# Kernel tuning notes

Hardware: AMD Instinct MI355X
Metric: run time of the kernel (lower is better)

## Reference

```python
import jax, jax.numpy as jnp
import numpy as np

B, N, DIM, H, DH = 8, 4096, 512, 8, 64
M = 266  # nb_features = int(dim_head * ln(dim_head)) = int(64*4.1589)
LN_EPS = 1e-5
K_EPS = 1e-4  # performer softmax_kernel epsilon


def _gaussian_orthogonal_matrix(m, d, rng):
    # performer_pytorch default: stacked QR blocks, rows scaled by chi(d) norms
    blocks = []
    n_full = m // d
    for _ in range(n_full):
        q, _ = np.linalg.qr(rng.standard_normal((d, d)))
        blocks.append(q.T)
    rem = m - n_full * d
    if rem > 0:
        q, _ = np.linalg.qr(rng.standard_normal((d, d)))
        blocks.append(q.T[:rem])
    proj = np.concatenate(blocks, axis=0)
    norms = np.linalg.norm(rng.standard_normal((m, d)), axis=1)
    return (proj * norms[:, None]).astype(np.float32)


def setup_inputs() -> dict:
    key = jax.random.key(0)
    ks = jax.random.split(key, 8)
    s_in = 1.0 / np.sqrt(DIM)
    s_ff = 1.0 / np.sqrt(4 * DIM)
    rng = np.random.default_rng(0)
    return {
        "x": jax.random.normal(ks[0], (B, N, DIM), jnp.float32),
        "w_q": jax.random.normal(ks[1], (DIM, DIM), jnp.float32) * s_in,
        "w_k": jax.random.normal(ks[2], (DIM, DIM), jnp.float32) * s_in,
        "w_v": jax.random.normal(ks[3], (DIM, DIM), jnp.float32) * s_in,
        "w_o": jax.random.normal(ks[4], (DIM, DIM), jnp.float32) * s_in,
        "b_o": jnp.zeros((DIM,), jnp.float32),
        "ln1_g": jnp.ones((DIM,), jnp.float32),
        "ln1_b": jnp.zeros((DIM,), jnp.float32),
        "ln2_g": jnp.ones((DIM,), jnp.float32),
        "ln2_b": jnp.zeros((DIM,), jnp.float32),
        "ff_w1": jax.random.normal(ks[5], (DIM, 4 * DIM), jnp.float32) * s_in,
        "ff_b1": jnp.zeros((4 * DIM,), jnp.float32),
        "ff_w2": jax.random.normal(ks[6], (4 * DIM, DIM), jnp.float32) * s_ff,
        "ff_b2": jnp.zeros((DIM,), jnp.float32),
        "projection": jnp.asarray(_gaussian_orthogonal_matrix(M, DH, rng)),
    }


def _layernorm(x, g, b):
    mu = jnp.mean(x, -1, keepdims=True)
    var = jnp.mean((x - mu) ** 2, -1, keepdims=True)
    return (x - mu) * jax.lax.rsqrt(var + LN_EPS) * g + b


def _softmax_kernel(data, proj, is_query):
    # FAVOR+ positive softmax-kernel features (performer_pytorch.softmax_kernel)
    dn = data.shape[-1] ** -0.25  # data_normalizer
    ratio = proj.shape[0] ** -0.5
    dd = jnp.einsum("bhnd,md->bhnm", data * dn, proj)
    diag = jnp.sum(data ** 2, -1, keepdims=True) * 0.5 * (dn ** 2)  # [B,H,N,1]
    if is_query:
        mx = jax.lax.stop_gradient(jnp.max(dd, -1, keepdims=True))
    else:
        mx = jax.lax.stop_gradient(jnp.max(dd))
    return ratio * (jnp.exp(dd - diag - mx) + K_EPS)


def reference(x, w_q, w_k, w_v, w_o, b_o, ln1_g, ln1_b, ln2_g, ln2_b,
              ff_w1, ff_b1, ff_w2, ff_b2, projection):
    # --- attention sublayer (pre-norm) ---
    h = _layernorm(x, ln1_g, ln1_b)

    def split_heads(t):
        return t.reshape(B, N, H, DH).transpose(0, 2, 1, 3)  # [B,H,N,DH]

    q = split_heads(h @ w_q)
    k = split_heads(h @ w_k)
    v = split_heads(h @ w_v)

    qp = _softmax_kernel(q, projection, True)   # [B,H,N,M]
    kp = _softmax_kernel(k, projection, False)  # [B,H,N,M]

    # non-causal linear attention: O(N) in sequence length
    d_inv = 1.0 / jnp.einsum("bhnm,bhm->bhn", qp, jnp.sum(kp, axis=2))
    ctx = jnp.einsum("bhnm,bhnd->bhmd", kp, v)          # [B,H,M,DH]
    attn = jnp.einsum("bhnm,bhmd,bhn->bhnd", qp, ctx, d_inv)
    attn = attn.transpose(0, 2, 1, 3).reshape(B, N, DIM)
    x = x + attn @ w_o + b_o

    # --- feed-forward sublayer (pre-norm) ---
    h2 = _layernorm(x, ln2_g, ln2_b)
    ff = jax.nn.gelu(h2 @ ff_w1 + ff_b1, approximate=False) @ ff_w2 + ff_b2
    return x + ff
```

## Files before the change

kernel.cpp:

```cpp
#include <hip/hip_runtime.h>
#include <cmath>

typedef unsigned short u16;
typedef unsigned int u32;
typedef short bf16x8 __attribute__((ext_vector_type(8)));
typedef float f32x4 __attribute__((ext_vector_type(4)));

#define DEVI __device__ __forceinline__

constexpr int NSEQ = 4096, DIMM = 512;
constexpr int KVLD = 1024;
constexpr int MP = 288;
constexpr int MPP = 296;
constexpr int MREAL = 266;
constexpr int DHP = 96;
constexpr float LNEPS = 1e-5f;
constexpr float KEPS = 1e-4f;
constexpr float DN = 0.3535533905932738f;
constexpr float HALF_DN2 = 0.0625f;

DEVI u16 f2bf(float f) {
  u32 u = __float_as_uint(f);
  u32 r = (u + 0x7FFFu + ((u >> 16) & 1u)) >> 16;
  return (u16)r;
}
DEVI float bf2f(u16 h) { return __uint_as_float(((u32)h) << 16); }

DEVI f32x4 mfma16(bf16x8 a, bf16x8 b, f32x4 c) {
  return __builtin_amdgcn_mfma_f32_16x16x32_bf16(a, b, c, 0, 0, 0);
}

DEVI void gload_lds16(const void* g, void* l) {
  __builtin_amdgcn_global_load_lds(
      (const __attribute__((address_space(1))) u32*)g,
      (__attribute__((address_space(3))) u32*)l, 16, 0, 0);
}

DEVI float gelu_fast(float z) {
  float a = fminf(1.5957691216057308f * (z + 0.044715f * z * z * z), 60.f);
  float e = __expf(a);
  return z * e * __builtin_amdgcn_rcpf(e + 1.f);
}

__global__ void ws_sentinel(float* out) { out[0] = 12345.0f; }

__launch_bounds__(256)
__global__ void transpose_cvt(const float* __restrict__ in, u16* __restrict__ out,
                              int K, int Nn) {
  __shared__ float tl[32][33];
  int ntn = Nn >> 5;
  int bid = blockIdx.x;
  int kt = bid / ntn, ntt = bid - kt * ntn;
  int k0 = kt << 5, nn0 = ntt << 5;
  int t = threadIdx.x;
  int r = t >> 5, c = t & 31;
#pragma unroll
  for (int i = 0; i < 4; ++i)
    tl[r + i * 8][c] = in[(size_t)(k0 + r + i * 8) * Nn + nn0 + c];
  __syncthreads();
#pragma unroll
  for (int i = 0; i < 4; ++i)
    out[(size_t)(nn0 + r + i * 8) * K + k0 + c] = f2bf(tl[c][r + i * 8]);
}

__global__ void proj_prep(const float* __restrict__ proj, u16* __restrict__ projf) {
  int idx = blockIdx.x * 256 + threadIdx.x;
  if (idx >= MP * 64) return;
  int e = idx & 7, lane = (idx >> 3) & 63, fh = idx >> 9;
  int f = fh >> 1, half = fh & 1;
  int m = f * 16 + (lane & 15);
  int d = half * 32 + (lane >> 4) * 8 + e;
  float v = (m < MREAL) ? proj[m * 64 + d] * DN : 0.f;
  projf[idx] = f2bf(v);
}

__launch_bounds__(256)
__global__ void ln_fwd(const float* __restrict__ x, const float* __restrict__ g,
                       const float* __restrict__ bt, u16* __restrict__ out) {
  int w = threadIdx.x >> 6, lane = threadIdx.x & 63;
  int row = blockIdx.x * 4 + w;
  const float* xr = x + (size_t)row * DIMM;
  int c0 = lane * 4;
  float4 v0 = *(const float4*)(xr + c0);
  float4 v1 = *(const float4*)(xr + 256 + c0);
  float s = v0.x + v0.y + v0.z + v0.w + v1.x + v1.y + v1.z + v1.w;
  float sq = v0.x * v0.x + v0.y * v0.y + v0.z * v0.z + v0.w * v0.w +
             v1.x * v1.x + v1.y * v1.y + v1.z * v1.z + v1.w * v1.w;
#pragma unroll
  for (int mk = 1; mk < 64; mk <<= 1) {
    s += __shfl_xor(s, mk, 64);
    sq += __shfl_xor(sq, mk, 64);
  }
  float mu = s * (1.f / 512.f);
  float var = sq * (1.f / 512.f) - mu * mu;
  float rstd = rsqrtf(var + LNEPS);
  float4 g0 = *(const float4*)(g + c0);
  float4 g1 = *(const float4*)(g + 256 + c0);
  float4 b0 = *(const float4*)(bt + c0);
  float4 b1 = *(const float4*)(bt + 256 + c0);
  u16* orow = out + (size_t)row * DIMM;
  uint2 p0, p1;
  {
    u16 h0 = f2bf((v0.x - mu) * rstd * g0.x + b0.x);
    u16 h1 = f2bf((v0.y - mu) * rstd * g0.y + b0.y);
    u16 h2 = f2bf((v0.z - mu) * rstd * g0.z + b0.z);
    u16 h3 = f2bf((v0.w - mu) * rstd * g0.w + b0.w);
    p0.x = ((u32)h1 << 16) | h0; p0.y = ((u32)h3 << 16) | h2;
  }
  {
    u16 h0 = f2bf((v1.x - mu) * rstd * g1.x + b1.x);
    u16 h1 = f2bf((v1.y - mu) * rstd * g1.y + b1.y);
    u16 h2 = f2bf((v1.z - mu) * rstd * g1.z + b1.z);
    u16 h3 = f2bf((v1.w - mu) * rstd * g1.w + b1.w);
    p1.x = ((u32)h1 << 16) | h0; p1.y = ((u32)h3 << 16) | h2;
  }
  *(uint2*)(orow + c0) = p0;
  *(uint2*)(orow + 256 + c0) = p1;
}

#define WAITVM(N) asm volatile("s_waitcnt vmcnt(" #N ")" ::: "memory")

template <int EPI>
__launch_bounds__(512)
__global__ void gemm256(const u16* __restrict__ A, int lda,
                        const u16* __restrict__ Bt, int ldb, int K,
                        void* __restrict__ OutP, int Nout, int ldo,
                        const float* __restrict__ bias,
                        const float* __restrict__ Res) {
  __shared__ __align__(16) u16 Al[2][256 * 64];
  __shared__ __align__(16) u16 Bl[2][256 * 64];
  int ntiles = Nout >> 8;
  int nwg = gridDim.x;
  int bid = blockIdx.x;
  int cpx = nwg >> 3;
  int wg = (bid & 7) * cpx + (bid >> 3);
  int mt = wg / ntiles, nt = wg - mt * ntiles;
  int t = threadIdx.x, lane = t & 63, w = t >> 6;
  int wm = w >> 2, wn = w & 3;
  int fr = lane & 15, fq = lane >> 4;
  int rowA0 = mt * 256, colB0 = nt * 256;
  int swz = (fr & 7) << 4;

  f32x4 acc[8][4];
#pragma unroll
  for (int i = 0; i < 8; ++i)
#pragma unroll
    for (int j = 0; j < 4; ++j) acc[i][j] = f32x4{0.f, 0.f, 0.f, 0.f};

  int srow = t >> 3;
  int so = ((t * 16) & 127) ^ ((srow & 7) << 4);

#define STAGE_G(bufi, k0)                                                       \
  do {                                                                          \
    _Pragma("unroll") for (int it = 0; it < 4; ++it) {                          \
      gload_lds16(                                                              \
          (const char*)(A + ((size_t)(rowA0 + srow + it * 64) * lda + (k0))) + so, \
          (char*)Al[bufi] + t * 16 + it * 8192);                                \
      gload_lds16(                                                              \
          (const char*)(Bt + ((size_t)(colB0 + srow + it * 64) * ldb + (k0))) + so, \
          (char*)Bl[bufi] + t * 16 + it * 8192);                                \
    }                                                                           \
  } while (0)

  int NT = K >> 6;
  STAGE_G(0, 0);
  STAGE_G(1, 64);
  int bi = 0;
  for (int tt = 0; tt < NT; ++tt) {
    if (tt + 1 < NT) { WAITVM(8); } else { WAITVM(0); }
    __builtin_amdgcn_s_barrier();

    bf16x8 av[8][2], bv[4][2];
#pragma unroll
    for (int i = 0; i < 8; ++i)
#pragma unroll
      for (int ks = 0; ks < 2; ++ks) {
        int row = wm * 128 + i * 16 + fr;
        av[i][ks] = *(const bf16x8*)((const char*)Al[bi] + row * 128 +
                                     (((ks << 6) | (fq << 4)) ^ swz));
      }
#pragma unroll
    for (int j = 0; j < 4; ++j)
#pragma unroll
      for (int ks = 0; ks < 2; ++ks) {
        int row = wn * 64 + (j)*16 + fr;
        bv[j][ks] = *(const bf16x8*)((const char*)Bl[bi] + row * 128 +
                                     (((ks << 6) | (fq << 4)) ^ swz));
      }

    __builtin_amdgcn_s_setprio(1);
#pragma unroll
    for (int i = 0; i < 4; ++i)
#pragma unroll
      for (int j = 0; j < 4; ++j)
#pragma unroll
        for (int ks = 0; ks < 2; ++ks)
          acc[i][j] = mfma16(av[i][ks], bv[j][ks], acc[i][j]);
    __builtin_amdgcn_s_setprio(0);

    asm volatile("s_waitcnt lgkmcnt(0)" ::: "memory");
    __builtin_amdgcn_sched_barrier(0);
    __builtin_amdgcn_s_barrier();
    if (tt + 2 < NT) STAGE_G(bi, (tt + 2) * 64);

    __builtin_amdgcn_s_setprio(1);
#pragma unroll
    for (int i = 4; i < 8; ++i)
#pragma unroll
      for (int j = 0; j < 4; ++j)
#pragma unroll
        for (int ks = 0; ks < 2; ++ks)
          acc[i][j] = mfma16(av[i][ks], bv[j][ks], acc[i][j]);
    __builtin_amdgcn_s_setprio(0);
    bi ^= 1;
  }
#undef STAGE_G

#pragma unroll
  for (int i = 0; i < 8; ++i)
#pragma unroll
    for (int j = 0; j < 4; ++j) {
      int row = rowA0 + wm * 128 + i * 16 + fq * 4;
      int col = colB0 + wn * 64 + j * 16 + fr;
#pragma unroll
      for (int r = 0; r < 4; ++r) {
        float v = acc[i][j][r];
        size_t idx = (size_t)(row + r) * ldo + col;
        if constexpr (EPI == 0) {
          ((u16*)OutP)[idx] = f2bf(v);
        } else if constexpr (EPI == 1) {
          ((float*)OutP)[idx] = v + bias[col] + Res[(size_t)(row + r) * 512 + col];
        } else if constexpr (EPI == 2) {
          ((u16*)OutP)[idx] = f2bf(gelu_fast(v + bias[col]));
        } else {
          float bb = bias ? bias[col] : 0.f;
          ((float*)OutP)[idx] += v + bb;
        }
      }
    }
}

__launch_bounds__(256)
__global__ void kmax_kernel(const u16* __restrict__ kv, const u16* __restrict__ projf,
                            u32* __restrict__ maxslot) {
  __shared__ float wred[4];
  int bid = blockIdx.x;
  int bh = bid >> 6, nt = bid & 63;
  int b = bh >> 3, h = bh & 7;
  int n0 = nt * 64;
  int t = threadIdx.x, lane = t & 63, w = t >> 6;
  int fr = lane & 15, fq = lane >> 4;

  const u16* krow = kv + ((size_t)(b * NSEQ + n0 + w * 16 + fr)) * KVLD + h * 64;
  bf16x8 a0 = *(const bf16x8*)(krow + fq * 8);
  bf16x8 a1 = *(const bf16x8*)(krow + 32 + fq * 8);

  const bf16x8* pf = (const bf16x8*)projf;
  float m = -1e30f;
#pragma unroll
  for (int f = 0; f < 18; ++f) {
    bf16x8 b0 = pf[(f * 2 + 0) * 64 + lane];
    bf16x8 b1 = pf[(f * 2 + 1) * 64 + lane];
    f32x4 z = {0.f, 0.f, 0.f, 0.f};
    z = mfma16(a0, b0, z);
    z = mfma16(a1, b1, z);
    if (f * 16 + fr < MREAL) {
#pragma unroll
      for (int r = 0; r < 4; ++r) m = fmaxf(m, z[r]);
    }
  }
#pragma unroll
  for (int mk = 1; mk < 64; mk <<= 1) m = fmaxf(m, __shfl_xor(m, mk, 64));
  if (lane == 0) wred[w] = m;
  __syncthreads();
  if (t == 0) {
    float mm = fmaxf(fmaxf(wred[0], wred[1]), fmaxf(wred[2], wred[3]));
    u32 u = __float_as_uint(mm);
    u32 enc = (u & 0x80000000u) ? ~u : (u | 0x80000000u);
    atomicMax(maxslot, enc);
  }
}

__launch_bounds__(512)
__global__ void fused_ctx(const u16* __restrict__ kvbuf, const u16* __restrict__ projf,
                          const u32* __restrict__ maxslot, float* __restrict__ part) {
  __shared__ __align__(16) u16 kt[64 * 64];
  __shared__ __align__(16) u16 kpL[MP * 64];
  __shared__ __align__(16) u16 vL[DHP * 64];
  int bid = blockIdx.x;
  int bh = bid >> 2, s = bid & 3;
  int b = bh >> 3, h = bh & 7;
  int t = threadIdx.x, lane = t & 63, w = t >> 6;
  int fr = lane & 15, fq = lane >> 4;
  int rg = w & 3, fh = w >> 2;
  int wq4 = w >> 1, wn = w & 1;
  int i_base = (wq4 < 2) ? wq4 * 5 : 10 + (wq4 - 2) * 4;
  int i_cnt = (wq4 < 2) ? 5 : 4;

  if (t < 256) {
    int rr = 64 + (t >> 3), sg = t & 7;
    u16 val = (rr == 64) ? (u16)0x3F80 : (u16)0;
    uint4 v4; u16* pv = (u16*)&v4;
#pragma unroll
    for (int e = 0; e < 8; ++e) pv[e] = val;
    *(uint4*)(vL + rr * 64 + sg * 8) = v4;
  }
  u32 enc = *maxslot;
  float gmax = __uint_as_float((enc & 0x80000000u) ? (enc & 0x7FFFFFFFu) : ~enc);
  const bf16x8* pf = (const bf16x8*)projf;

  f32x4 acc[5][3];
#pragma unroll
  for (int i = 0; i < 5; ++i)
#pragma unroll
    for (int j = 0; j < 3; ++j) acc[i][j] = f32x4{0.f, 0.f, 0.f, 0.f};

  int str = t >> 3;
  int sch = (t & 7) ^ (str & 7);

  for (int tile = 0; tile < 16; ++tile) {
    int n0 = s * 1024 + tile * 64;
    gload_lds16(kvbuf + ((size_t)(b * NSEQ + n0 + str)) * KVLD + h * 64 + sch * 8,
                (char*)kt + t * 16);
#pragma unroll
    for (int it = 0; it < 2; ++it) {
      int idx = t + it * 512;
      int r = idx >> 4, sg = idx & 15;
      uint2 val = *(const uint2*)(kvbuf + ((size_t)(b * NSEQ + n0 + r)) * KVLD + 512 + h * 64 + sg * 4);
      u16* pv = (u16*)&val;
#pragma unroll
      for (int e = 0; e < 4; ++e) {
        int d = sg * 4 + e;
        int ch = (r >> 3) ^ (d & 7);
        ((u16*)((char*)vL + d * 128 + ch * 16))[r & 7] = pv[e];
      }
    }
    __syncthreads();

    float dg[4];
#pragma unroll
    for (int r4 = 0; r4 < 4; ++r4) {
      int row = rg * 16 + fq * 4 + r4;
      int ch = (fr >> 1) ^ (row & 7);
      const u16* kr = (const u16*)((const char*)kt + row * 128 + ch * 16) + (fr & 1) * 4;
      float ssum = 0.f;
#pragma unroll
      for (int e = 0; e < 4; ++e) { float xv = bf2f(kr[e]); ssum += xv * xv; }
#pragma unroll
      for (int mk = 1; mk < 16; mk <<= 1) ssum += __shfl_xor(ssum, mk, 64);
      dg[r4] = ssum * HALF_DN2;
    }
    int rowa = rg * 16 + fr;
    bf16x8 a0 = *(const bf16x8*)((const char*)kt + rowa * 128 +
                                 ((fq ^ (fr & 7)) << 4));
    bf16x8 a1 = *(const bf16x8*)((const char*)kt + rowa * 128 +
                                 (((4 + fq) ^ (fr & 7)) << 4));
#pragma unroll
    for (int ff = 0; ff < 9; ++ff) {
      int f = fh * 9 + ff;
      bf16x8 b0 = pf[(f * 2 + 0) * 64 + lane];
      bf16x8 b1 = pf[(f * 2 + 1) * 64 + lane];
      f32x4 z = {0.f, 0.f, 0.f, 0.f};
      z = mfma16(a0, b0, z);
      z = mfma16(a1, b1, z);
      int col = f * 16 + fr;
      bool ok = col < MREAL;
      float k0v = ok ? (__expf(z[0] - dg[0] - gmax) + KEPS) : 0.f;
      float k1v = ok ? (__expf(z[1] - dg[1] - gmax) + KEPS) : 0.f;
      float k2v = ok ? (__expf(z[2] - dg[2] - gmax) + KEPS) : 0.f;
      float k3v = ok ? (__expf(z[3] - dg[3] - gmax) + KEPS) : 0.f;
      u32 lo, hi;
      asm("v_cvt_pk_bf16_f32 %0, %1, %2" : "=v"(lo) : "v"(k0v), "v"(k1v));
      asm("v_cvt_pk_bf16_f32 %0, %1, %2" : "=v"(hi) : "v"(k2v), "v"(k3v));
      uint2 pk2; pk2.x = lo; pk2.y = hi;
      int ch = (rg * 2 + (fq >> 1)) ^ (fr & 7);
      *(uint2*)((char*)kpL + col * 128 + ch * 16 + (fq & 1) * 8) = pk2;
    }
    __syncthreads();

#pragma unroll
    for (int kc = 0; kc < 2; ++kc) {
      int rch = ((kc * 4 + fq) ^ (fr & 7)) << 4;
      bf16x8 av[5], bv[3];
#pragma unroll
      for (int i = 0; i < 5; ++i)
        if (i < i_cnt)
          av[i] = *(const bf16x8*)((const char*)kpL + ((i_base + i) * 16 + fr) * 128 + rch);
#pragma unroll
      for (int j = 0; j < 3; ++j)
        bv[j] = *(const bf16x8*)((const char*)vL + (wn * 48 + j * 16 + fr) * 128 + rch);
#pragma unroll
      for (int i = 0; i < 5; ++i)
        if (i < i_cnt)
#pragma unroll
          for (int j = 0; j < 3; ++j) acc[i][j] = mfma16(av[i], bv[j], acc[i][j]);
    }
    __syncthreads();
  }

  float* dst = part + ((size_t)bh * 4 + s) * MP * DHP;
#pragma unroll
  for (int i = 0; i < 5; ++i)
    if (i < i_cnt)
#pragma unroll
      for (int j = 0; j < 3; ++j) {
        int m = (i_base + i) * 16 + fq * 4;
        int c = wn * 48 + j * 16 + fr;
#pragma unroll
        for (int r = 0; r < 4; ++r) dst[(size_t)(m + r) * DHP + c] = acc[i][j][r];
      }
}

__launch_bounds__(256)
__global__ void ctx_reduce2(const float* __restrict__ part, u16* __restrict__ ctxT) {
  int bh = blockIdx.x, t = threadIdx.x;
  const float* p = part + (size_t)bh * 4 * MP * DHP;
  u16* dst = ctxT + (size_t)bh * DHP * MP;
  for (int idx = t; idx < DHP * MP; idx += 256) {
    int d = idx / MP, m = idx - d * MP;
    size_t o = (size_t)m * DHP + d;
    float v = p[o] + p[o + MP * DHP] + p[o + 2 * MP * DHP] + p[o + 3 * MP * DHP];
    dst[idx] = f2bf(v);
  }
}

__launch_bounds__(256)
__global__ void fused_attn(const u16* __restrict__ qb, const u16* __restrict__ ctxT,
                           const u16* __restrict__ projf, u16* __restrict__ attnb) {
  __shared__ __align__(16) u16 qt[64 * 64];
  __shared__ __align__(16) u16 qpL[64 * MPP];
  __shared__ float dbuf[64];
  int bid = blockIdx.x;
  int bh = bid >> 6, nt = bid & 63;
  int b = bh >> 3, h = bh & 7;
  int n0 = nt * 64;
  int t = threadIdx.x, lane = t & 63, w = t >> 6;
  int wm = w >> 1, wn = w & 1;
  int fr = lane & 15, fq = lane >> 4;

#pragma unroll
  for (int it = 0; it < 4; ++it) {
    int idx = t + it * 256;
    int r = idx >> 4, sg = idx & 15;
    int dst = (r * 128 + sg * 8) ^ ((r & 7) << 4);
    *(uint2*)((char*)qt + dst) =
        *(const uint2*)(qb + ((size_t)(b * NSEQ + n0 + r)) * KVLD + h * 64 + sg * 4);
  }
  __syncthreads();

  int swz = (fr & 7) << 4;
  bf16x8 a0 = *(const bf16x8*)((const char*)qt +
                               (((w * 16 + fr) * 128 + fq * 16) ^ swz));
  bf16x8 a1 = *(const bf16x8*)((const char*)qt +
                               (((w * 16 + fr) * 128 + 64 + fq * 16) ^ swz));

  float ss = 0.f;
#pragma unroll
  for (int e = 0; e < 8; ++e) {
    float x0 = bf2f((u16)a0[e]), x1 = bf2f((u16)a1[e]);
    ss += x0 * x0 + x1 * x1;
  }
  ss += __shfl_xor(ss, 16, 64);
  ss += __shfl_xor(ss, 32, 64);
  float dg = ss * HALF_DN2;

  const bf16x8* pf = (const bf16x8*)projf;
  f32x4 accf[18];
#pragma unroll
  for (int f = 0; f < 18; ++f) {
    f32x4 z = {0.f, 0.f, 0.f, 0.f};
    z = mfma16(pf[(f * 2 + 0) * 64 + lane], a0, z);
    z = mfma16(pf[(f * 2 + 1) * 64 + lane], a1, z);
    accf[f] = z;
  }
  float mm = -1e30f;
#pragma unroll
  for (int f = 0; f < 18; ++f)
#pragma unroll
    for (int r = 0; r < 4; ++r) mm = fmaxf(mm, accf[f][r]);
  mm = fmaxf(mm, __shfl_xor(mm, 16, 64));
  mm = fmaxf(mm, __shfl_xor(mm, 32, 64));

  u16* qp = qpL + (w * 16 + fr) * MPP + fq * 4;
#pragma unroll
  for (int f = 0; f < 18; ++f) {
    float e0 = __expf(accf[f][0] - dg - mm) + KEPS;
    float e1 = __expf(accf[f][1] - dg - mm) + KEPS;
    float e2 = __expf(accf[f][2] - dg - mm) + KEPS;
    float e3 = __expf(accf[f][3] - dg - mm) + KEPS;
    u32 lo, hi;
    asm("v_cvt_pk_bf16_f32 %0, %1, %2" : "=v"(lo) : "v"(e0), "v"(e1));
    asm("v_cvt_pk_bf16_f32 %0, %1, %2" : "=v"(hi) : "v"(e2), "v"(e3));
    uint2 pk; pk.x = lo; pk.y = hi;
    *(uint2*)(qp + f * 16) = pk;
  }
  __syncthreads();

  const u16* cg = ctxT + (size_t)bh * DHP * MP;
  f32x4 acc2[2][3];
#pragma unroll
  for (int i = 0; i < 2; ++i)
#pragma unroll
    for (int j = 0; j < 3; ++j) acc2[i][j] = f32x4{0.f, 0.f, 0.f, 0.f};
  bf16x8 bvc[3];
#pragma unroll
  for (int j = 0; j < 3; ++j)
    bvc[j] = *(const bf16x8*)(cg + (size_t)(wn * 48 + j * 16 + fr) * MP + fq * 8);
#pragma unroll
  for (int kc = 0; kc < 9; ++kc) {
    bf16x8 bvn[3];
    if (kc < 8) {
#pragma unroll
      for (int j = 0; j < 3; ++j)
        bvn[j] = *(const bf16x8*)(cg + (size_t)(wn * 48 + j * 16 + fr) * MP +
                                  (kc + 1) * 32 + fq * 8);
    }
    bf16x8 av[2];
#pragma unroll
    for (int i = 0; i < 2; ++i)
      av[i] = *(const bf16x8*)(qpL + (wm * 32 + i * 16 + fr) * MPP + kc * 32 + fq * 8);
#pragma unroll
    for (int i = 0; i < 2; ++i)
#pragma unroll
      for (int j = 0; j < 3; ++j) acc2[i][j] = mfma16(av[i], bvc[j], acc2[i][j]);
    if (kc < 8) {
#pragma unroll
      for (int j = 0; j < 3; ++j) bvc[j] = bvn[j];
    }
  }
  if (wn == 1 && fr == 0) {
#pragma unroll
    for (int i = 0; i < 2; ++i) {
      int rl = wm * 32 + i * 16 + fq * 4;
#pragma unroll
      for (int r = 0; r < 4; ++r) dbuf[rl + r] = acc2[i][1][r];
    }
  }
  __syncthreads();

  u16* ob = qt;
#pragma unroll
  for (int i = 0; i < 2; ++i)
#pragma unroll
    for (int j = 0; j < 3; ++j) {
      int cl = wn * 48 + j * 16 + fr;
      if (cl < 64) {
        int rl = wm * 32 + i * 16 + fq * 4;
#pragma unroll
        for (int r = 0; r < 4; ++r)
          ob[(rl + r) * 64 + cl] = f2bf(acc2[i][j][r] / dbuf[rl + r]);
      }
    }
  __syncthreads();

  u16* dst = attnb + ((size_t)(b * NSEQ + n0)) * KVLD + h * 64;
  for (int idx = t; idx < 64 * 8; idx += 256) {
    int r = idx >> 3, sg = idx & 7;
    *(uint4*)(dst + (size_t)r * KVLD + sg * 8) = *(const uint4*)(ob + r * 64 + sg * 8);
  }
}

constexpr size_t OFF_WQT   = 0;
constexpr size_t OFF_WKT   = 524288;
constexpr size_t OFF_WVT   = 1048576;
constexpr size_t OFF_WOT   = 1572864;
constexpr size_t OFF_FF1T  = 2097152;
constexpr size_t OFF_FF2T  = 4194304;
constexpr size_t OFF_PROJF = 6328320;
constexpr size_t OFF_MAX   = 6365184;
constexpr size_t OFF_CTXT  = 6365440;
constexpr size_t OFF_H     = 9904384;
constexpr size_t OFF_KV    = 43458816;
constexpr size_t OFF_PART  = 110567680;
constexpr size_t WS_NEED   = 138879232;

extern "C" void kernel_launch(void* const* d_in, const int* in_sizes, int n_in,
                              void* d_out, int out_size, void* d_ws, size_t ws_size,
                              hipStream_t stream) {
  const float* x    = (const float*)d_in[0];
  const float* w_q  = (const float*)d_in[1];
  const float* w_k  = (const float*)d_in[2];
  const float* w_v  = (const float*)d_in[3];
  const float* w_o  = (const float*)d_in[4];
  const float* b_o  = (const float*)d_in[5];
  const float* ln1g = (const float*)d_in[6];
  const float* ln1b = (const float*)d_in[7];
  const float* ln2g = (const float*)d_in[8];
  const float* ln2b = (const float*)d_in[9];
  const float* ffw1 = (const float*)d_in[10];
  const float* ffb1 = (const float*)d_in[11];
  const float* ffw2 = (const float*)d_in[12];
  const float* ffb2 = (const float*)d_in[13];
  const float* proj = (const float*)d_in[14];
  (void)in_sizes; (void)n_in; (void)out_size;

  float* dout = (float*)d_out;
  if (ws_size < WS_NEED) {
    ws_sentinel<<<1, 1, 0, stream>>>(dout);
    return;
  }

  char* ws = (char*)d_ws;
  u16* wqt   = (u16*)(ws + OFF_WQT);
  u16* wkt   = (u16*)(ws + OFF_WKT);
  u16* wvt   = (u16*)(ws + OFF_WVT);
  u16* wot   = (u16*)(ws + OFF_WOT);
  u16* ff1t  = (u16*)(ws + OFF_FF1T);
  u16* ff2t  = (u16*)(ws + OFF_FF2T);
  u16* projf = (u16*)(ws + OFF_PROJF);
  u32* maxsl = (u32*)(ws + OFF_MAX);
  u16* ctxt  = (u16*)(ws + OFF_CTXT);
  u16* hbuf  = (u16*)(ws + OFF_H);
  u16* kvbuf = (u16*)(ws + OFF_KV);
  float* part = (float*)(ws + OFF_PART);

  hipMemsetAsync(maxsl, 0, 4, stream);

  transpose_cvt<<<256, 256, 0, stream>>>(w_q, wqt, 512, 512);
  transpose_cvt<<<256, 256, 0, stream>>>(w_k, wkt, 512, 512);
  transpose_cvt<<<256, 256, 0, stream>>>(w_v, wvt, 512, 512);
  transpose_cvt<<<256, 256, 0, stream>>>(w_o, wot, 512, 512);
  transpose_cvt<<<1024, 256, 0, stream>>>(ffw1, ff1t, 512, 2048);
  transpose_cvt<<<1024, 256, 0, stream>>>(ffw2, ff2t, 2048, 512);
  proj_prep<<<72, 256, 0, stream>>>(proj, projf);

  ln_fwd<<<8192, 256, 0, stream>>>(x, ln1g, ln1b, hbuf);
  gemm256<0><<<512, 512, 0, stream>>>(hbuf, 512, wkt, 512, 512, kvbuf, 1024, 1024, nullptr, nullptr);
  kmax_kernel<<<4096, 256, 0, stream>>>(kvbuf, projf, maxsl);
  fused_ctx<<<256, 512, 0, stream>>>(kvbuf, projf, maxsl, part);
  ctx_reduce2<<<64, 256, 0, stream>>>(part, ctxt);
  gemm256<0><<<256, 512, 0, stream>>>(hbuf, 512, wqt, 512, 512, kvbuf, 512, 1024, nullptr, nullptr);
  fused_attn<<<4096, 256, 0, stream>>>(kvbuf, ctxt, projf, kvbuf + 512);
  gemm256<1><<<256, 512, 0, stream>>>(kvbuf + 512, 1024, wot, 512, 512, dout, 512, 512, b_o, x);
  ln_fwd<<<8192, 256, 0, stream>>>(dout, ln2g, ln2b, hbuf);
  for (int c = 0; c < 2; ++c) {
    gemm256<2><<<512, 512, 0, stream>>>(hbuf, 512, ff1t + (size_t)c * 1024 * 512, 512, 512,
                                        kvbuf, 1024, 1024, ffb1 + c * 1024, nullptr);
    gemm256<3><<<256, 512, 0, stream>>>(kvbuf, 1024, ff2t + c * 1024, 2048, 1024,
                                        dout, 512, 512, (c == 0) ? ffb2 : nullptr, nullptr);
  }
}
```

Baseline: 614.6 us.

## Double-buffer K/V tile loads and hoist projection fragments in fused_ctx

The fused_ctx loop now double-buffers the K tile in LDS and prefetches the next tile's K (async global-to-LDS) and V (into registers) while the current tile is computed. The barriers become explicit lgkmcnt waits plus raw s_barrier. The projection-matrix fragments are loaded once into registers before the loop instead of every tile. The per-row squared norm is now computed from the already-loaded A fragments with shuffles instead of separate LDS reads. This hides global-load latency and removes redundant loads, at the cost of more registers and LDS, which may reduce occupancy.

```diff
diff --git a/kernel.cpp b/kernel.cpp
--- a/kernel.cpp
+++ b/kernel.cpp
@@ -284,7 +284,7 @@
 __launch_bounds__(512)
 __global__ void fused_ctx(const u16* __restrict__ kvbuf, const u16* __restrict__ projf,
                           const u32* __restrict__ maxslot, float* __restrict__ part) {
-  __shared__ __align__(16) u16 kt[64 * 64];
+  __shared__ __align__(16) u16 kt[2][64 * 64];
   __shared__ __align__(16) u16 kpL[MP * 64];
   __shared__ __align__(16) u16 vL[DHP * 64];
   int bid = blockIdx.x;
@@ -309,6 +309,13 @@
   float gmax = __uint_as_float((enc & 0x80000000u) ? (enc & 0x7FFFFFFFu) : ~enc);
   const bf16x8* pf = (const bf16x8*)projf;
 
+  bf16x8 pfr0[9], pfr1[9];
+#pragma unroll
+  for (int ff = 0; ff < 9; ++ff) {
+    pfr0[ff] = pf[((fh * 9 + ff) * 2 + 0) * 64 + lane];
+    pfr1[ff] = pf[((fh * 9 + ff) * 2 + 1) * 64 + lane];
+  }
+
   f32x4 acc[5][3];
 #pragma unroll
   for (int i = 0; i < 5; ++i)
@@ -317,58 +324,76 @@
 
   int str = t >> 3;
   int sch = (t & 7) ^ (str & 7);
+  int vr0 = t >> 4, vsg = t & 15;
+  uint2 vra, vrb;
+
+#define KT_LOAD(ci, n0)                                                        \
+  gload_lds16(kvbuf + ((size_t)(b * NSEQ + (n0) + str)) * KVLD + h * 64 + sch * 8, \
+              (char*)kt[ci] + t * 16)
+#define V_LOAD(n0)                                                             \
+  do {                                                                         \
+    vra = *(const uint2*)(kvbuf + ((size_t)(b * NSEQ + (n0) + vr0)) * KVLD + 512 + h * 64 + vsg * 4); \
+    vrb = *(const uint2*)(kvbuf + ((size_t)(b * NSEQ + (n0) + vr0 + 32)) * KVLD + 512 + h * 64 + vsg * 4); \
+  } while (0)
+
+  KT_LOAD(0, s * 1024);
+  V_LOAD(s * 1024);
+  int cur = 0;
 
   for (int tile = 0; tile < 16; ++tile) {
     int n0 = s * 1024 + tile * 64;
-    gload_lds16(kvbuf + ((size_t)(b * NSEQ + n0 + str)) * KVLD + h * 64 + sch * 8,
-                (char*)kt + t * 16);
-#pragma unroll
-    for (int it = 0; it < 2; ++it) {
-      int idx = t + it * 512;
-      int r = idx >> 4, sg = idx & 15;
-      uint2 val = *(const uint2*)(kvbuf + ((size_t)(b * NSEQ + n0 + r)) * KVLD + 512 + h * 64 + sg * 4);
-      u16* pv = (u16*)&val;
+    WAITVM(0);
+
+    {
+      u16* pv = (u16*)&vra;
 #pragma unroll
       for (int e = 0; e < 4; ++e) {
-        int d = sg * 4 + e;
-        int ch = (r >> 3) ^ (d & 7);
-        ((u16*)((char*)vL + d * 128 + ch * 16))[r & 7] = pv[e];
+        int d = vsg * 4 + e, ch = (vr0 >> 3) ^ (d & 7);
+        ((u16*)((char*)vL + d * 128 + ch * 16))[vr0 & 7] = pv[e];
       }
-    }
-    __syncthreads();
-
-    float dg[4];
-#pragma unroll
-    for (int r4 = 0; r4 < 4; ++r4) {
-      int row = rg * 16 + fq * 4 + r4;
-      int ch = (fr >> 1) ^ (row & 7);
-      const u16* kr = (const u16*)((const char*)kt + row * 128 + ch * 16) + (fr & 1) * 4;
-      float ssum = 0.f;
-#pragma unroll
-      for (int e = 0; e < 4; ++e) { float xv = bf2f(kr[e]); ssum += xv * xv; }
-#pragma unroll
-      for (int mk = 1; mk < 16; mk <<= 1) ssum += __shfl_xor(ssum, mk, 64);
-      dg[r4] = ssum * HALF_DN2;
-    }
+      u16* pw = (u16*)&vrb;
+      int r2 = vr0 + 32;
+#pragma unroll
+      for (int e = 0; e < 4; ++e) {
+        int d = vsg * 4 + e, ch = (r2 >> 3) ^ (d & 7);
+        ((u16*)((char*)vL + d * 128 + ch * 16))[r2 & 7] = pw[e];
+      }
+    }
+    if (tile < 15) { KT_LOAD(cur ^ 1, n0 + 64); V_LOAD(n0 + 64); }
+    asm volatile("s_waitcnt lgkmcnt(0)" ::: "memory");
+    __builtin_amdgcn_s_barrier();
+
     int rowa = rg * 16 + fr;
-    bf16x8 a0 = *(const bf16x8*)((const char*)kt + rowa * 128 +
+    bf16x8 a0 = *(const bf16x8*)((const char*)kt[cur] + rowa * 128 +
                                  ((fq ^ (fr & 7)) << 4));
-    bf16x8 a1 = *(const bf16x8*)((const char*)kt + rowa * 128 +
+    bf16x8 a1 = *(const bf16x8*)((const char*)kt[cur] + rowa * 128 +
                                  (((4 + fq) ^ (fr & 7)) << 4));
+
+    float ss = 0.f;
+#pragma unroll
+    for (int e = 0; e < 8; ++e) {
+      float x0 = bf2f((u16)a0[e]), x1 = bf2f((u16)a1[e]);
+      ss += x0 * x0 + x1 * x1;
+    }
+    ss += __shfl_xor(ss, 16, 64);
+    ss += __shfl_xor(ss, 32, 64);
+    float dgv[4];
+#pragma unroll
+    for (int r4 = 0; r4 < 4; ++r4)
+      dgv[r4] = __shfl(ss, fq * 4 + r4, 64) * HALF_DN2;
+
 #pragma unroll
     for (int ff = 0; ff < 9; ++ff) {
       int f = fh * 9 + ff;
-      bf16x8 b0 = pf[(f * 2 + 0) * 64 + lane];
-      bf16x8 b1 = pf[(f * 2 + 1) * 64 + lane];
       f32x4 z = {0.f, 0.f, 0.f, 0.f};
-      z = mfma16(a0, b0, z);
-      z = mfma16(a1, b1, z);
+      z = mfma16(a0, pfr0[ff], z);
+      z = mfma16(a1, pfr1[ff], z);
       int col = f * 16 + fr;
       bool ok = col < MREAL;
-      float k0v = ok ? (__expf(z[0] - dg[0] - gmax) + KEPS) : 0.f;
-      float k1v = ok ? (__expf(z[1] - dg[1] - gmax) + KEPS) : 0.f;
-      float k2v = ok ? (__expf(z[2] - dg[2] - gmax) + KEPS) : 0.f;
-      float k3v = ok ? (__expf(z[3] - dg[3] - gmax) + KEPS) : 0.f;
+      float k0v = ok ? (__expf(z[0] - dgv[0] - gmax) + KEPS) : 0.f;
+      float k1v = ok ? (__expf(z[1] - dgv[1] - gmax) + KEPS) : 0.f;
+      float k2v = ok ? (__expf(z[2] - dgv[2] - gmax) + KEPS) : 0.f;
+      float k3v = ok ? (__expf(z[3] - dgv[3] - gmax) + KEPS) : 0.f;
       u32 lo, hi;
       asm("v_cvt_pk_bf16_f32 %0, %1, %2" : "=v"(lo) : "v"(k0v), "v"(k1v));
       asm("v_cvt_pk_bf16_f32 %0, %1, %2" : "=v"(hi) : "v"(k2v), "v"(k3v));
@@ -376,7 +401,8 @@
       int ch = (rg * 2 + (fq >> 1)) ^ (fr & 7);
       *(uint2*)((char*)kpL + col * 128 + ch * 16 + (fq & 1) * 8) = pk2;
     }
-    __syncthreads();
+    asm volatile("s_waitcnt lgkmcnt(0)" ::: "memory");
+    __builtin_amdgcn_s_barrier();
 
 #pragma unroll
     for (int kc = 0; kc < 2; ++kc) {
@@ -395,8 +421,12 @@
 #pragma unroll
           for (int j = 0; j < 3; ++j) acc[i][j] = mfma16(av[i], bv[j], acc[i][j]);
     }
-    __syncthreads();
-  }
+    asm volatile("s_waitcnt lgkmcnt(0)" ::: "memory");
+    __builtin_amdgcn_s_barrier();
+    cur ^= 1;
+  }
+#undef KT_LOAD
+#undef V_LOAD
 
   float* dst = part + ((size_t)bh * 4 + s) * MP * DHP;
 #pragma unroll
```

New measurement: 601.2 us. -2.2%, faster.
